# Optimization experiments

Hardware: AMD Instinct MI355X
Metric: run time of the kernel (lower is better)

The kernel has to match this reference:

```python
import jax, jax.numpy as jnp
import numpy as np
import math

B, CF, H, W = 2, 64, 256, 256
CH = 32          # 'channel' init arg
KS, DIL, PAD = 3, 2, 2
IMG_H, IMG_W = 512, 512


def _pos_encode(h, w, d_model):
    # Sinusoidal encoding along x and y, interleaved sin/cos -> [2*d_model, h, w]
    div = jnp.exp(jnp.arange(0, d_model, 2, dtype=jnp.float32) * (-math.log(10000.0) / d_model))  # [d/2]
    ax = jnp.arange(w, dtype=jnp.float32)[None, :] * div[:, None]   # [d/2, w]
    ay = jnp.arange(h, dtype=jnp.float32)[None, :] * div[:, None]   # [d/2, h]
    x = jnp.stack([jnp.sin(ax), jnp.cos(ax)], axis=1).reshape(d_model, w)  # even=sin, odd=cos
    y = jnp.stack([jnp.sin(ay), jnp.cos(ay)], axis=1).reshape(d_model, h)
    x = jnp.broadcast_to(x[:, None, :], (d_model, h, w))
    y = jnp.broadcast_to(y[:, :, None], (d_model, h, w))
    return jnp.concatenate([x, y], axis=0)  # [2*d_model, h, w]


def _unfold3x3(x):
    # F.unfold(kernel=3, dilation=2, padding=2, stride=1) -> [B, C, 9, H, W]
    b, c, h, w = x.shape
    xp = jnp.pad(x, ((0, 0), (0, 0), (PAD, PAD), (PAD, PAD)))
    offs = (0, DIL, 2 * DIL)
    patches = [xp[:, :, i:i + h, j:j + w] for i in offs for j in offs]  # row-major kernel order
    return jnp.stack(patches, axis=2)


def setup_inputs() -> dict:
    key = jax.random.key(0)
    k1, k2, k3, k4, k5 = jax.random.split(key, 5)
    return {
        "inp": jax.random.normal(k1, (B, CF, H, W), dtype=jnp.float32),
        "img": jax.random.uniform(k2, (B, 3, IMG_H, IMG_W), dtype=jnp.float32),
        "w_pos": jax.random.normal(k3, (CH, 2 * CH), dtype=jnp.float32) * 0.1,
        "w_img": jax.random.normal(k4, (CH, 3), dtype=jnp.float32) * 0.1,
        "w_comp": jax.random.normal(k5, (CF,), dtype=jnp.float32) * 0.1,
    }


def reference(inp, img, w_pos, w_img, w_comp):
    b, cf, h, w = inp.shape
    # positional embedding -> 1x1 conv (channel matmul)
    pos = _pos_encode(h, w, CH)                                   # [2*CH, H, W]
    pos_embd = jnp.einsum('oc,chw->ohw', w_pos, pos)              # [CH, H, W]
    pos_embd = jnp.broadcast_to(pos_embd[None], (b, CH, h, w))
    # bilinear resize of image to feature resolution, then 1x1 conv
    rimg = jax.image.resize(img, (b, 3, h, w), method='bilinear')
    rimg = jnp.einsum('oc,bchw->bohw', w_img, rimg)               # [B, CH, H, W]
    em = jnp.concatenate([rimg, pos_embd], axis=1)                # [B, 2*CH, H, W]
    # neighborhood similarity score
    un_em = _unfold3x3(em)                                        # [B, 2CH, 9, H, W]
    feature_score = jnp.einsum('bckhw,bchw->bkhw', un_em, em)     # [B, 9, H, W]
    # feature compatibility: 1x1 conv (dot with w_comp) per neighbor, sigmoid
    un_fea = _unfold3x3(inp)                                      # [B, CF, 9, H, W]
    comp_score = jax.nn.sigmoid(jnp.einsum('bckhw,c->bkhw', un_fea, w_comp))
    phi = comp_score * feature_score                              # [B, 9, H, W]
    weighted_fea = jnp.einsum('bckhw,bkhw->bchw', un_fea, phi)    # [B, CF, H, W]
    return weighted_fea
```

## Files before the change

### kernel.cpp

```cpp
#include <hip/hip_runtime.h>
#include <math.h>

namespace {
constexpr int Bn = 2, CF = 64, CHN = 32;
constexpr int H = 256, W = 256, HW = H * W;
constexpr int IH = 512, IW = 512;

constexpr int OFF_MT   = 0;
constexpr int OFF_GXX  = OFF_MT + 256 * 256;
constexpr int OFF_GYY  = OFF_GXX + 3 * 256;
constexpr int OFF_EM   = OFF_GYY + 3 * 256;
constexpr int OFF_S    = OFF_EM + Bn * CHN * HW;
constexpr int OFF_PHI  = OFF_S + Bn * HW;
constexpr int OFF_RIMG = OFF_PHI + Bn * 9 * HW;
constexpr int OFF_PX   = OFF_EM;
constexpr int OFF_PY   = OFF_EM + 32 * 256;
}

__global__ __launch_bounds__(256) void pxy_kernel(
    const float* __restrict__ w_pos,
    float* __restrict__ PX, float* __restrict__ PY)
{
  const int t = threadIdx.x;
  const int o = blockIdx.x;
  float s[16], c[16];
#pragma unroll
  for (int i = 0; i < 16; i++) {
    float d = expf((float)(2 * i) * (-0.2878231366242557f));
    float a = (float)t * d;
    s[i] = sinf(a);
    c[i] = cosf(a);
  }
  const float* wr = w_pos + o * 64;
  float ax = 0.f, ay = 0.f;
#pragma unroll
  for (int i = 0; i < 16; i++) {
    ax += wr[2 * i] * s[i] + wr[2 * i + 1] * c[i];
    ay += wr[32 + 2 * i] * s[i] + wr[33 + 2 * i] * c[i];
  }
  PX[o * 256 + t] = ax;
  PY[o * 256 + t] = ay;
}

__global__ __launch_bounds__(256) void gram_kernel(
    const float* __restrict__ PX, const float* __restrict__ PY,
    float* __restrict__ Mt, float* __restrict__ GXX, float* __restrict__ GYY)
{
  const int a = threadIdx.x;
  const int t = blockIdx.x;

  float m = 0.f;
#pragma unroll
  for (int o = 0; o < 32; o++) m += PX[o * 256 + a] * PY[o * 256 + t];
  Mt[t * 256 + a] = m;

  if (t == 0) {
#pragma unroll
    for (int j = 0; j < 3; j++) {
      const int nb = a + 2 * (j - 1);
      float gx = 0.f, gy = 0.f;
      if (nb >= 0 && nb < 256) {
#pragma unroll
        for (int o = 0; o < 32; o++) {
          gx += PX[o * 256 + a] * PX[o * 256 + nb];
          gy += PY[o * 256 + a] * PY[o * 256 + nb];
        }
      }
      GXX[j * 256 + a] = gx;
      GYY[j * 256 + a] = gy;
    }
  }
}

__device__ __forceinline__ void resize_taps(int p, int n, float w[4], int idx[4])
{
#pragma unroll
  for (int r = 0; r < 4; r++) {
    int q = 2 * p - 1 + r;
    idx[r] = min(max(q, 0), 2 * n - 1);
  }
  if (p == 0)          { w[0] = 0.f;        w[1] = 3.f / 7.f; w[2] = 3.f / 7.f; w[3] = 1.f / 7.f; }
  else if (p == n - 1) { w[0] = 1.f / 7.f;  w[1] = 3.f / 7.f; w[2] = 3.f / 7.f; w[3] = 0.f; }
  else                 { w[0] = 0.125f;     w[1] = 0.375f;    w[2] = 0.375f;    w[3] = 0.125f; }
}

__global__ __launch_bounds__(256) void rimg_kernel(
    const float* __restrict__ img, float* __restrict__ rimg)
{
  const int p = blockIdx.x * 256 + threadIdx.x;
  const int c = blockIdx.y;
  const int b = blockIdx.z;
  const int x = p & (W - 1);
  const int y = p >> 8;

  float wy[4], wx[4];
  int ry[4], rx[4];
  resize_taps(y, H, wy, ry);
  resize_taps(x, W, wx, rx);

  const float* ip = img + ((size_t)(b * 3 + c) * IH) * IW;
  float acc = 0.f;
#pragma unroll
  for (int r = 0; r < 4; r++) {
    const float* rowp = ip + ry[r] * IW;
    float rs = wx[0] * rowp[rx[0]] + wx[1] * rowp[rx[1]] +
               wx[2] * rowp[rx[2]] + wx[3] * rowp[rx[3]];
    acc += wy[r] * rs;
  }
  rimg[((size_t)(b * 3 + c)) * HW + p] = acc;
}

__global__ __launch_bounds__(256) void em_proj_kernel(
    const float* __restrict__ rimg, const float* __restrict__ w_img,
    float* __restrict__ em)
{
  const int p = blockIdx.x * 256 + threadIdx.x;
  const int oq = blockIdx.y;
  const int b = blockIdx.z;
  const float r0 = rimg[((size_t)(b * 3 + 0)) * HW + p];
  const float r1 = rimg[((size_t)(b * 3 + 1)) * HW + p];
  const float r2 = rimg[((size_t)(b * 3 + 2)) * HW + p];
  float* eb = em + (size_t)b * CHN * HW;
#pragma unroll
  for (int i = 0; i < 4; i++) {
    const int o = oq * 4 + i;
    eb[(size_t)o * HW + p] =
        w_img[o * 3] * r0 + w_img[o * 3 + 1] * r1 + w_img[o * 3 + 2] * r2;
  }
}

__global__ __launch_bounds__(256) void smap_kernel(
    const float* __restrict__ inp, const float* __restrict__ w_comp,
    float* __restrict__ smap)
{
  __shared__ float red[256];
  const int lane = threadIdx.x & 63;
  const int cg = threadIdx.x >> 6;
  const int p = blockIdx.x * 64 + lane;
  const int b = blockIdx.z;

  const float* ib = inp + (size_t)b * CF * HW + (size_t)cg * 16 * HW + p;
  float a0 = 0.f, a1 = 0.f, a2 = 0.f, a3 = 0.f;
#pragma unroll
  for (int c = 0; c < 16; c += 4) {
    a0 += ib[(size_t)(c + 0) * HW] * w_comp[cg * 16 + c + 0];
    a1 += ib[(size_t)(c + 1) * HW] * w_comp[cg * 16 + c + 1];
    a2 += ib[(size_t)(c + 2) * HW] * w_comp[cg * 16 + c + 2];
    a3 += ib[(size_t)(c + 3) * HW] * w_comp[cg * 16 + c + 3];
  }
  red[threadIdx.x] = (a0 + a1) + (a2 + a3);
  __syncthreads();
  if (threadIdx.x < 64) {
    smap[(size_t)b * HW + blockIdx.x * 64 + threadIdx.x] =
        red[threadIdx.x] + red[threadIdx.x + 64] +
        red[threadIdx.x + 128] + red[threadIdx.x + 192];
  }
}

__global__ __launch_bounds__(256) void phi_kernel(
    const float* __restrict__ em, const float* __restrict__ smap,
    const float* __restrict__ Mt, const float* __restrict__ GXX,
    const float* __restrict__ GYY, float* __restrict__ phi)
{
  const int p = blockIdx.x * 256 + threadIdx.x;
  const int k = blockIdx.y;
  const int b = blockIdx.z;
  const int x = p & (W - 1);
  const int y = p >> 8;
  const int ky = k / 3, kx = k % 3;
  const int ny = y + 2 * (ky - 1), nx = x + 2 * (kx - 1);
  const bool valid = ((unsigned)ny < (unsigned)H) & ((unsigned)nx < (unsigned)W);
  const int cy = min(max(ny, 0), H - 1);
  const int cx = min(max(nx, 0), W - 1);
  const int np = cy * W + cx;

  const float* eb = em + (size_t)b * CHN * HW;
  float a0 = 0.f, a1 = 0.f, a2 = 0.f, a3 = 0.f;
#pragma unroll
  for (int c = 0; c < CHN; c += 4) {
    a0 += eb[(size_t)(c + 0) * HW + p] * eb[(size_t)(c + 0) * HW + np];
    a1 += eb[(size_t)(c + 1) * HW + p] * eb[(size_t)(c + 1) * HW + np];
    a2 += eb[(size_t)(c + 2) * HW + p] * eb[(size_t)(c + 2) * HW + np];
    a3 += eb[(size_t)(c + 3) * HW + p] * eb[(size_t)(c + 3) * HW + np];
  }
  float fs = (a0 + a1) + (a2 + a3);
  fs += GXX[kx * 256 + x] + GYY[ky * 256 + y] + Mt[y * 256 + cx] + Mt[cy * 256 + x];

  const float s = smap[(size_t)b * HW + np];
  const float cs = 1.f / (1.f + expf(-s));
  phi[((size_t)(b * 9 + k)) * HW + p] = valid ? cs * fs : 0.f;
}

__global__ __launch_bounds__(256) void gather_kernel(
    const float* __restrict__ inp, const float* __restrict__ phi,
    float* __restrict__ out)
{
  const int cg = blockIdx.x;
  const int p = blockIdx.y * 256 + threadIdx.x;
  const int b = blockIdx.z;
  const int x = p & (W - 1);
  const int y = p >> 8;

  float ph[9];
  int nb[9];
#pragma unroll
  for (int k = 0; k < 9; k++) {
    const int ky = k / 3, kx = k % 3;
    const int ny = y + 2 * (ky - 1), nx = x + 2 * (kx - 1);
    const int cy = min(max(ny, 0), H - 1);
    const int cx = min(max(nx, 0), W - 1);
    nb[k] = cy * W + cx;
    ph[k] = phi[((size_t)(b * 9 + k)) * HW + p];
  }

  const float* ib = inp + (size_t)b * CF * HW + (size_t)cg * 4 * HW;
  float* ob = out + (size_t)b * CF * HW + (size_t)cg * 4 * HW;
#pragma unroll
  for (int c = 0; c < 4; c++) {
    const float* ic = ib + (size_t)c * HW;
    float acc = ph[0] * ic[nb[0]];
#pragma unroll
    for (int k = 1; k < 9; k++) acc += ph[k] * ic[nb[k]];
    ob[(size_t)c * HW + p] = acc;
  }
}

extern "C" void kernel_launch(void* const* d_in, const int* in_sizes, int n_in,
                              void* d_out, int out_size, void* d_ws, size_t ws_size,
                              hipStream_t stream)
{
  const float* inp    = (const float*)d_in[0];
  const float* img    = (const float*)d_in[1];
  const float* w_pos  = (const float*)d_in[2];
  const float* w_img  = (const float*)d_in[3];
  const float* w_comp = (const float*)d_in[4];
  float* out = (float*)d_out;
  float* ws  = (float*)d_ws;

  float* Mt   = ws + OFF_MT;
  float* GXX  = ws + OFF_GXX;
  float* GYY  = ws + OFF_GYY;
  float* em   = ws + OFF_EM;
  float* smap = ws + OFF_S;
  float* phi  = ws + OFF_PHI;
  float* rimg = ws + OFF_RIMG;
  float* PX   = ws + OFF_PX;
  float* PY   = ws + OFF_PY;

  hipLaunchKernelGGL(pxy_kernel, dim3(32), dim3(256), 0, stream, w_pos, PX, PY);
  hipLaunchKernelGGL(gram_kernel, dim3(256), dim3(256), 0, stream,
                     PX, PY, Mt, GXX, GYY);

  hipLaunchKernelGGL(rimg_kernel, dim3(HW / 256, 3, Bn), dim3(256), 0, stream,
                     img, rimg);
  hipLaunchKernelGGL(em_proj_kernel, dim3(HW / 256, 8, Bn), dim3(256), 0, stream,
                     rimg, w_img, em);
  hipLaunchKernelGGL(smap_kernel, dim3(HW / 64, 1, Bn), dim3(256), 0, stream,
                     inp, w_comp, smap);

  hipLaunchKernelGGL(phi_kernel, dim3(HW / 256, 9, Bn), dim3(256), 0, stream,
                     em, smap, Mt, GXX, GYY, phi);

  hipLaunchKernelGGL(gather_kernel, dim3(CF / 4, HW / 256, Bn), dim3(256), 0, stream,
                     inp, phi, out);
}
```

Before: 140.5 us.

## Replace 32-channel image embedding dot product with 3x3 Gram form

Drops the em_proj kernel that materialized the 32-channel projected image embedding. The image part of the neighborhood similarity is now computed as r^T (W^T W) n, using a 3x3 Gram matrix of w_img built once in gram_kernel. phi_kernel then reads 6 rimg values per pixel instead of 64 em values, which removes a large write and read of intermediate data and one launch. Floating-point summation order changes, so results may differ slightly in rounding.

```diff
diff --git a/kernel.cpp b/kernel.cpp
--- a/kernel.cpp
+++ b/kernel.cpp
@@ -2,19 +2,19 @@
 #include <math.h>
 
 namespace {
-constexpr int Bn = 2, CF = 64, CHN = 32;
+constexpr int Bn = 2, CF = 64;
 constexpr int H = 256, W = 256, HW = H * W;
 constexpr int IH = 512, IW = 512;
 
 constexpr int OFF_MT   = 0;
 constexpr int OFF_GXX  = OFF_MT + 256 * 256;
 constexpr int OFF_GYY  = OFF_GXX + 3 * 256;
-constexpr int OFF_EM   = OFF_GYY + 3 * 256;
-constexpr int OFF_S    = OFF_EM + Bn * CHN * HW;
+constexpr int OFF_G    = OFF_GYY + 3 * 256;
+constexpr int OFF_RIMG = OFF_G + 16;
+constexpr int OFF_S    = OFF_RIMG + Bn * 3 * HW;
 constexpr int OFF_PHI  = OFF_S + Bn * HW;
-constexpr int OFF_RIMG = OFF_PHI + Bn * 9 * HW;
-constexpr int OFF_PX   = OFF_EM;
-constexpr int OFF_PY   = OFF_EM + 32 * 256;
+constexpr int OFF_PX   = OFF_RIMG;
+constexpr int OFF_PY   = OFF_RIMG + 32 * 256;
 }
 
 __global__ __launch_bounds__(256) void pxy_kernel(
@@ -44,7 +44,9 @@
 
 __global__ __launch_bounds__(256) void gram_kernel(
     const float* __restrict__ PX, const float* __restrict__ PY,
-    float* __restrict__ Mt, float* __restrict__ GXX, float* __restrict__ GYY)
+    const float* __restrict__ w_img,
+    float* __restrict__ Mt, float* __restrict__ GXX, float* __restrict__ GYY,
+    float* __restrict__ G)
 {
   const int a = threadIdx.x;
   const int t = blockIdx.x;
@@ -69,6 +71,13 @@
       GXX[j * 256 + a] = gx;
       GYY[j * 256 + a] = gy;
     }
+    if (a < 9) {
+      const int i = a / 3, j = a % 3;
+      float g = 0.f;
+#pragma unroll
+      for (int o = 0; o < 32; o++) g += w_img[o * 3 + i] * w_img[o * 3 + j];
+      G[a] = g;
+    }
   }
 }
 
@@ -108,25 +117,6 @@
     acc += wy[r] * rs;
   }
   rimg[((size_t)(b * 3 + c)) * HW + p] = acc;
-}
-
-__global__ __launch_bounds__(256) void em_proj_kernel(
-    const float* __restrict__ rimg, const float* __restrict__ w_img,
-    float* __restrict__ em)
-{
-  const int p = blockIdx.x * 256 + threadIdx.x;
-  const int oq = blockIdx.y;
-  const int b = blockIdx.z;
-  const float r0 = rimg[((size_t)(b * 3 + 0)) * HW + p];
-  const float r1 = rimg[((size_t)(b * 3 + 1)) * HW + p];
-  const float r2 = rimg[((size_t)(b * 3 + 2)) * HW + p];
-  float* eb = em + (size_t)b * CHN * HW;
-#pragma unroll
-  for (int i = 0; i < 4; i++) {
-    const int o = oq * 4 + i;
-    eb[(size_t)o * HW + p] =
-        w_img[o * 3] * r0 + w_img[o * 3 + 1] * r1 + w_img[o * 3 + 2] * r2;
-  }
 }
 
 __global__ __launch_bounds__(256) void smap_kernel(
@@ -158,9 +148,10 @@
 }
 
 __global__ __launch_bounds__(256) void phi_kernel(
-    const float* __restrict__ em, const float* __restrict__ smap,
+    const float* __restrict__ rimg, const float* __restrict__ smap,
     const float* __restrict__ Mt, const float* __restrict__ GXX,
-    const float* __restrict__ GYY, float* __restrict__ phi)
+    const float* __restrict__ GYY, const float* __restrict__ G,
+    float* __restrict__ phi)
 {
   const int p = blockIdx.x * 256 + threadIdx.x;
   const int k = blockIdx.y;
@@ -174,16 +165,17 @@
   const int cx = min(max(nx, 0), W - 1);
   const int np = cy * W + cx;
 
-  const float* eb = em + (size_t)b * CHN * HW;
-  float a0 = 0.f, a1 = 0.f, a2 = 0.f, a3 = 0.f;
-#pragma unroll
-  for (int c = 0; c < CHN; c += 4) {
-    a0 += eb[(size_t)(c + 0) * HW + p] * eb[(size_t)(c + 0) * HW + np];
-    a1 += eb[(size_t)(c + 1) * HW + p] * eb[(size_t)(c + 1) * HW + np];
-    a2 += eb[(size_t)(c + 2) * HW + p] * eb[(size_t)(c + 2) * HW + np];
-    a3 += eb[(size_t)(c + 3) * HW + p] * eb[(size_t)(c + 3) * HW + np];
-  }
-  float fs = (a0 + a1) + (a2 + a3);
+  const float* rb = rimg + (size_t)b * 3 * HW;
+  const float r0 = rb[p],            r1 = rb[HW + p],      r2 = rb[2 * HW + p];
+  const float n0 = rb[np],           n1 = rb[HW + np],     n2 = rb[2 * HW + np];
+
+  const float g0 = G[0], g1 = G[1], g2 = G[2];
+  const float g3 = G[3], g4 = G[4], g5 = G[5];
+  const float g6 = G[6], g7 = G[7], g8 = G[8];
+
+  float fs = r0 * (g0 * n0 + g1 * n1 + g2 * n2)
+           + r1 * (g3 * n0 + g4 * n1 + g5 * n2)
+           + r2 * (g6 * n0 + g7 * n1 + g8 * n2);
   fs += GXX[kx * 256 + x] + GYY[ky * 256 + y] + Mt[y * 256 + cx] + Mt[cy * 256 + x];
 
   const float s = smap[(size_t)b * HW + np];
@@ -240,26 +232,24 @@
   float* Mt   = ws + OFF_MT;
   float* GXX  = ws + OFF_GXX;
   float* GYY  = ws + OFF_GYY;
-  float* em   = ws + OFF_EM;
+  float* G    = ws + OFF_G;
+  float* rimg = ws + OFF_RIMG;
   float* smap = ws + OFF_S;
   float* phi  = ws + OFF_PHI;
-  float* rimg = ws + OFF_RIMG;
   float* PX   = ws + OFF_PX;
   float* PY   = ws + OFF_PY;
 
   hipLaunchKernelGGL(pxy_kernel, dim3(32), dim3(256), 0, stream, w_pos, PX, PY);
   hipLaunchKernelGGL(gram_kernel, dim3(256), dim3(256), 0, stream,
-                     PX, PY, Mt, GXX, GYY);
+                     PX, PY, w_img, Mt, GXX, GYY, G);
 
   hipLaunchKernelGGL(rimg_kernel, dim3(HW / 256, 3, Bn), dim3(256), 0, stream,
                      img, rimg);
-  hipLaunchKernelGGL(em_proj_kernel, dim3(HW / 256, 8, Bn), dim3(256), 0, stream,
-                     rimg, w_img, em);
   hipLaunchKernelGGL(smap_kernel, dim3(HW / 64, 1, Bn), dim3(256), 0, stream,
                      inp, w_comp, smap);
 
   hipLaunchKernelGGL(phi_kernel, dim3(HW / 256, 9, Bn), dim3(256), 0, stream,
-                     em, smap, Mt, GXX, GYY, phi);
+                     rimg, smap, Mt, GXX, GYY, G, phi);
 
   hipLaunchKernelGGL(gather_kernel, dim3(CF / 4, HW / 256, Bn), dim3(256), 0, stream,
                      inp, phi, out);
```

Result: faster. 125.1 us (-10.9%).
